# Optimization experiments

Hardware: AMD Instinct MI355X
Metric: run time of the kernel (lower is better)

Reference implementation:

```python
import jax, jax.numpy as jnp
import numpy as np

OUT_FEATURES = 4096
IN_FEATURES = 4096
GROUP_SIZE = 128
N_GROUPS = OUT_FEATURES * IN_FEATURES // GROUP_SIZE  # 131072


def setup_inputs() -> dict:
    key = jax.random.key(0)
    k_x, k_t, k_s = jax.random.split(key, 3)
    x = jax.random.normal(k_x, (4, 2048, IN_FEATURES), dtype=jnp.float32)
    # ternary codes in {-1, 0, 1}, stored as int (int8 in the original module)
    ternary = jax.random.randint(k_t, (OUT_FEATURES, IN_FEATURES), 0, 3, dtype=jnp.int32) - 1
    # per-group positive scales (beta = mean |w| per group in the original init)
    scales = jax.random.uniform(k_s, (N_GROUPS,), dtype=jnp.float32, minval=0.01, maxval=0.1)
    return {"x": x, "ternary": ternary, "scales": scales}


def reference(x, ternary, scales):
    # Dequantize: expand per-group scale across group_size, multiply ternary sign.
    w = (ternary.astype(jnp.float32).reshape(-1, GROUP_SIZE) * scales[:, None])
    w = w.reshape(OUT_FEATURES, IN_FEATURES)
    # F.linear(x, W) = x @ W.T
    return jnp.einsum('bsi,oi->bso', x, w)
```

## Files before the change

kernel.cpp:

```cpp
#include <hip/hip_runtime.h>
#include <hip/hip_bf16.h>


#define Msz 8192
#define Nsz 4096
#define Ksz 4096

typedef __attribute__((ext_vector_type(8))) short short8;
typedef __attribute__((ext_vector_type(4))) float f32x4;
typedef __attribute__((ext_vector_type(4))) int int4v;
typedef __attribute__((ext_vector_type(4))) float float4v;
typedef __attribute__((ext_vector_type(8))) unsigned short ushort8;

static __device__ __forceinline__ unsigned short f2bf(float f) {
    unsigned u = __builtin_bit_cast(unsigned, f);
    u += 0x7fffu + ((u >> 16) & 1u);
    return (unsigned short)(u >> 16);
}

__global__ void prep(const float* __restrict__ x, const int* __restrict__ t,
                     const float* __restrict__ s,
                     unsigned short* __restrict__ ox, unsigned short* __restrict__ ow) {
    if (blockIdx.x < 2048) {
        int i = blockIdx.x * 256 + threadIdx.x;
        for (; i < Msz * Ksz / 8; i += 2048 * 256) {
            const float4v* p = (const float4v*)x + (size_t)i * 2;
            float4v a = p[0], b = p[1];
            ushort8 r;
            r[0] = f2bf(a[0]); r[1] = f2bf(a[1]); r[2] = f2bf(a[2]); r[3] = f2bf(a[3]);
            r[4] = f2bf(b[0]); r[5] = f2bf(b[1]); r[6] = f2bf(b[2]); r[7] = f2bf(b[3]);
            *((ushort8*)ox + i) = r;
        }
    } else {
        int i = (blockIdx.x - 2048) * 256 + threadIdx.x;
        for (; i < Nsz * Ksz / 8; i += 1024 * 256) {
            float sc = s[i >> 4];
            const int4v* p = (const int4v*)t + (size_t)i * 2;
            int4v a = p[0], b = p[1];
            ushort8 r;
            r[0] = f2bf((float)a[0] * sc); r[1] = f2bf((float)a[1] * sc);
            r[2] = f2bf((float)a[2] * sc); r[3] = f2bf((float)a[3] * sc);
            r[4] = f2bf((float)b[0] * sc); r[5] = f2bf((float)b[1] * sc);
            r[6] = f2bf((float)b[2] * sc); r[7] = f2bf((float)b[3] * sc);
            *((ushort8*)ow + i) = r;
        }
    }
}


#define READ_B(b) {                                                              \
    _Pragma("unroll") for (int n = 0; n < 4; ++n)                                \
    _Pragma("unroll") for (int ks = 0; ks < 2; ++ks)                             \
      bfr[n][ks] = *(const short8*)(L + (b)*65536 + 32768 + ((((wc)*4+n)*2+ks)<<10) + laneA); }

#define READ_A(b, q) {                                                           \
    _Pragma("unroll") for (int m = 0; m < 2; ++m)                                \
    _Pragma("unroll") for (int ks = 0; ks < 2; ++ks)                             \
      af[m][ks] = *(const short8*)(L + (b)*65536 + ((((q)*4+(wr)*2+m)*2+ks)<<10) + laneA); }

#define MFMAS(q) {                                                               \
    _Pragma("unroll") for (int m = 0; m < 2; ++m)                                \
    _Pragma("unroll") for (int n = 0; n < 4; ++n) {                              \
      acc[(q)*2+m][n] = __builtin_amdgcn_mfma_f32_16x16x32_bf16(af[m][0], bfr[n][0], acc[(q)*2+m][n], 0, 0, 0); \
      acc[(q)*2+m][n] = __builtin_amdgcn_mfma_f32_16x16x32_bf16(af[m][1], bfr[n][1], acc[(q)*2+m][n], 0, 0, 0); } }

#define STAGE_H(PM, MOFF, BOFF, T, H) {                                          \
    _Pragma("unroll") for (int j = 0; j < 2; ++j)                                \
      __builtin_amdgcn_global_load_lds(                                          \
        (const __attribute__((address_space(1))) void*)(PM + (size_t)((H)*128 + j*64)*Ksz + (T)*64), \
        (__attribute__((address_space(3))) void*)(L + (BOFF) + (MOFF) + (H)*16384 + j*8192 + dOff), \
        16, 0, 0); }

#define WAITV8  asm volatile("s_waitcnt vmcnt(8)"  ::: "memory");
#define WAITV10 asm volatile("s_waitcnt vmcnt(10)" ::: "memory");

#define PHASE(READS, QM, STG, WV)                                                \
    READS;                                                                       \
    STG;                                                                         \
    __builtin_amdgcn_sched_barrier(0);                                           \
    __builtin_amdgcn_s_barrier();                                                \
    asm volatile("s_waitcnt lgkmcnt(0)" ::: "memory");                           \
    __builtin_amdgcn_sched_barrier(0);                                           \
    __builtin_amdgcn_s_setprio(1);                                               \
    MFMAS(QM);                                                                   \
    __builtin_amdgcn_s_setprio(0);                                               \
    WV;                                                                          \
    __builtin_amdgcn_sched_barrier(0);                                           \
    __builtin_amdgcn_s_barrier();                                                \
    __builtin_amdgcn_sched_barrier(0);

__global__ __launch_bounds__(512, 2) void gemm_8p(const unsigned short* __restrict__ A,
                                                  const unsigned short* __restrict__ B,
                                                  float* __restrict__ C) {
    __shared__ __align__(16) unsigned char L[131072];

    const int tid  = threadIdx.x;
    const int lane = tid & 63;
    const int wid  = tid >> 6;
    const int wr   = wid >> 2;
    const int wc   = wid & 3;
    const int rowBase = blockIdx.y * 256;
    const int colBase = blockIdx.x * 256;

    const int laneA = (((lane & 15) * 64) + ((lane >> 4) * 16)) ^ (((lane >> 3) & 1) << 5);
    const int kloc = (lane & 1) * 8 + (((lane >> 1) ^ (lane >> 5)) & 1) * 16;
    const int r_st = lane >> 2;
    const int dOff = wid * 1024;

    const unsigned short* pAb = A + (size_t)(rowBase + (wid >> 1) * 16 + r_st) * Ksz + (wid & 1) * 32 + kloc;
    const unsigned short* pBb = B + (size_t)(colBase + (wid >> 1) * 16 + r_st) * Ksz + (wid & 1) * 32 + kloc;

    f32x4 acc[8][4] = {};
    short8 af[2][2], bfr[4][2];

    STAGE_H(pBb, 32768, 0,     0, 0);
    STAGE_H(pAb, 0,     0,     0, 0);
    STAGE_H(pBb, 32768, 0,     0, 1);
    STAGE_H(pAb, 0,     0,     0, 1);
    STAGE_H(pBb, 32768, 65536, 1, 0);
    STAGE_H(pAb, 0,     65536, 1, 1);
    STAGE_H(pBb, 32768, 65536, 1, 1);
    WAITV8
    __builtin_amdgcn_sched_barrier(0);
    __builtin_amdgcn_s_barrier();
    __builtin_amdgcn_sched_barrier(0);

    for (int i = 0; i < 32; ++i) {
        const int t1 = 2 * i + 1;
        const int t2 = (i < 31) ? 2 * i + 2 : 62;
        const int t3 = (i < 31) ? 2 * i + 3 : 62;

        PHASE({ READ_B(0); READ_A(0, 0); }, 0, STAGE_H(pAb, 0,     65536, t1, 0), )
        PHASE(READ_A(0, 1),                 1, STAGE_H(pBb, 32768, 0,     t2, 0), WAITV10)
        PHASE(READ_A(0, 2),                 2, STAGE_H(pAb, 0,     0,     t2, 0), )
        PHASE(READ_A(0, 3),                 3, STAGE_H(pBb, 32768, 0,     t2, 1), WAITV8)
        PHASE({ READ_B(1); READ_A(1, 2); }, 2, STAGE_H(pAb, 0,     0,     t2, 1), )
        PHASE(READ_A(1, 3),                 3, STAGE_H(pBb, 32768, 65536, t3, 0), WAITV10)
        PHASE(READ_A(1, 0),                 0, STAGE_H(pAb, 0,     65536, t3, 1), )
        PHASE(READ_A(1, 1),                 1, STAGE_H(pBb, 32768, 65536, t3, 1), WAITV8)
    }

    asm volatile("s_waitcnt vmcnt(0)" ::: "memory");

    const int crl = (lane >> 4) * 4;
    const int ccol0 = colBase + wc * 64 + (lane & 15);
#pragma unroll
    for (int q = 0; q < 4; ++q)
#pragma unroll
        for (int m = 0; m < 2; ++m)
#pragma unroll
            for (int n = 0; n < 4; ++n) {
                const int row0 = rowBase + (q * 4 + wr * 2 + m) * 16 + crl;
                float* cp = C + (size_t)row0 * Nsz + ccol0 + n * 16;
#pragma unroll
                for (int j = 0; j < 4; ++j)
                    cp[(size_t)j * Nsz] = acc[q * 2 + m][n][j];
            }
}

__global__ void gemm_naive(const float* __restrict__ x, const int* __restrict__ t,
                           const float* __restrict__ s, float* __restrict__ C) {
    size_t o = (size_t)blockIdx.x * blockDim.x + threadIdx.x;
    if (o >= (size_t)Msz * Nsz) return;
    int m = (int)(o / Nsz), n = (int)(o % Nsz);
    float acc = 0.f;
    for (int g = 0; g < Ksz / 128; ++g) {
        float sc = s[n * (Ksz / 128) + g];
        float p = 0.f;
        const float* xp = x + (size_t)m * Ksz + g * 128;
        const int* tp = t + (size_t)n * Ksz + g * 128;
        for (int k = 0; k < 128; ++k) p += xp[k] * (float)tp[k];
        acc += sc * p;
    }
    C[o] = acc;
}

extern "C" void kernel_launch(void* const* d_in, const int* in_sizes, int n_in,
                              void* d_out, int out_size, void* d_ws, size_t ws_size,
                              hipStream_t stream) {
    const float* x      = (const float*)d_in[0];
    const int*   tern   = (const int*)d_in[1];
    const float* scales = (const float*)d_in[2];
    float* out = (float*)d_out;

    const size_t aBytes = (size_t)Msz * Ksz * 2;
    const size_t bBytes = (size_t)Nsz * Ksz * 2;

    if (ws_size >= aBytes + bBytes) {
        unsigned short* Abf = (unsigned short*)d_ws;
        unsigned short* Bbf = (unsigned short*)((char*)d_ws + aBytes);
        prep<<<3072, 256, 0, stream>>>(x, tern, scales, Abf, Bbf);
        dim3 grid(Nsz / 256, Msz / 256);
        gemm_8p<<<grid, 512, 0, stream>>>(Abf, Bbf, out);
    } else {
        gemm_naive<<<(int)(((size_t)Msz * Nsz + 255) / 256), 256, 0, stream>>>(x, tern, scales, out);
    }
}
```

Before: 266.0 us.

## Double-buffer LDS fragment registers to overlap LDS reads with MFMAs

Splits the A and B fragment registers into even and odd sets, so each phase issues the LDS reads for the next phase while running MFMAs on fragments loaded in the previous phase. The full lgkmcnt(0) wait becomes a partial lgkmcnt wait, and a prologue preloads the first fragments. The goal is to hide LDS read latency behind matrix math. It costs more VGPRs, which could hurt occupancy at launch bounds (512,2). The partial counts also make correctness depend on the vmcnt/lgkmcnt ordering and on the reordered staging slots staying right.

```diff
diff --git a/kernel.cpp b/kernel.cpp
--- a/kernel.cpp
+++ b/kernel.cpp
@@ -48,21 +48,21 @@
 }
 
 
-#define READ_B(b) {                                                              \
+#define READ_B_TO(S, b) {                                                        \
     _Pragma("unroll") for (int n = 0; n < 4; ++n)                                \
     _Pragma("unroll") for (int ks = 0; ks < 2; ++ks)                             \
-      bfr[n][ks] = *(const short8*)(L + (b)*65536 + 32768 + ((((wc)*4+n)*2+ks)<<10) + laneA); }
-
-#define READ_A(b, q) {                                                           \
+      S[n][ks] = *(const short8*)(L + (b)*65536 + 32768 + ((((wc)*4+n)*2+ks)<<10) + laneA); }
+
+#define READ_A_TO(S, b, q) {                                                     \
     _Pragma("unroll") for (int m = 0; m < 2; ++m)                                \
     _Pragma("unroll") for (int ks = 0; ks < 2; ++ks)                             \
-      af[m][ks] = *(const short8*)(L + (b)*65536 + ((((q)*4+(wr)*2+m)*2+ks)<<10) + laneA); }
-
-#define MFMAS(q) {                                                               \
+      S[m][ks] = *(const short8*)(L + (b)*65536 + ((((q)*4+(wr)*2+m)*2+ks)<<10) + laneA); }
+
+#define MFMAS_X(q, AF, BF) {                                                     \
     _Pragma("unroll") for (int m = 0; m < 2; ++m)                                \
     _Pragma("unroll") for (int n = 0; n < 4; ++n) {                              \
-      acc[(q)*2+m][n] = __builtin_amdgcn_mfma_f32_16x16x32_bf16(af[m][0], bfr[n][0], acc[(q)*2+m][n], 0, 0, 0); \
-      acc[(q)*2+m][n] = __builtin_amdgcn_mfma_f32_16x16x32_bf16(af[m][1], bfr[n][1], acc[(q)*2+m][n], 0, 0, 0); } }
+      acc[(q)*2+m][n] = __builtin_amdgcn_mfma_f32_16x16x32_bf16(AF[m][0], BF[n][0], acc[(q)*2+m][n], 0, 0, 0); \
+      acc[(q)*2+m][n] = __builtin_amdgcn_mfma_f32_16x16x32_bf16(AF[m][1], BF[n][1], acc[(q)*2+m][n], 0, 0, 0); } }
 
 #define STAGE_H(PM, MOFF, BOFF, T, H) {                                          \
     _Pragma("unroll") for (int j = 0; j < 2; ++j)                                \
@@ -73,16 +73,18 @@
 
 #define WAITV8  asm volatile("s_waitcnt vmcnt(8)"  ::: "memory");
 #define WAITV10 asm volatile("s_waitcnt vmcnt(10)" ::: "memory");
-
-#define PHASE(READS, QM, STG, WV)                                                \
+#define LG4  asm volatile("s_waitcnt lgkmcnt(4)"  ::: "memory");
+#define LG12 asm volatile("s_waitcnt lgkmcnt(12)" ::: "memory");
+
+#define PHASEP(READS, MF, STG, LG, WV)                                           \
     READS;                                                                       \
     STG;                                                                         \
     __builtin_amdgcn_sched_barrier(0);                                           \
     __builtin_amdgcn_s_barrier();                                                \
-    asm volatile("s_waitcnt lgkmcnt(0)" ::: "memory");                           \
+    LG;                                                                          \
     __builtin_amdgcn_sched_barrier(0);                                           \
     __builtin_amdgcn_s_setprio(1);                                               \
-    MFMAS(QM);                                                                   \
+    MF;                                                                          \
     __builtin_amdgcn_s_setprio(0);                                               \
     WV;                                                                          \
     __builtin_amdgcn_sched_barrier(0);                                           \
@@ -111,7 +113,7 @@
     const unsigned short* pBb = B + (size_t)(colBase + (wid >> 1) * 16 + r_st) * Ksz + (wid & 1) * 32 + kloc;
 
     f32x4 acc[8][4] = {};
-    short8 af[2][2], bfr[4][2];
+    short8 afE[2][2], afO[2][2], bfrE[4][2], bfrO[4][2];
 
     STAGE_H(pBb, 32768, 0,     0, 0);
     STAGE_H(pAb, 0,     0,     0, 0);
@@ -125,22 +127,28 @@
     __builtin_amdgcn_s_barrier();
     __builtin_amdgcn_sched_barrier(0);
 
+    READ_B_TO(bfrE, 0);
+    READ_A_TO(afE, 0, 0);
+    STAGE_H(pAb, 0, 65536, 1, 0);
+    __builtin_amdgcn_sched_barrier(0);
+    __builtin_amdgcn_s_barrier();
+    __builtin_amdgcn_sched_barrier(0);
+
     for (int i = 0; i < 32; ++i) {
-        const int t1 = 2 * i + 1;
         const int t2 = (i < 31) ? 2 * i + 2 : 62;
         const int t3 = (i < 31) ? 2 * i + 3 : 62;
 
-        PHASE({ READ_B(0); READ_A(0, 0); }, 0, STAGE_H(pAb, 0,     65536, t1, 0), )
-        PHASE(READ_A(0, 1),                 1, STAGE_H(pBb, 32768, 0,     t2, 0), WAITV10)
-        PHASE(READ_A(0, 2),                 2, STAGE_H(pAb, 0,     0,     t2, 0), )
-        PHASE(READ_A(0, 3),                 3, STAGE_H(pBb, 32768, 0,     t2, 1), WAITV8)
-        PHASE({ READ_B(1); READ_A(1, 2); }, 2, STAGE_H(pAb, 0,     0,     t2, 1), )
-        PHASE(READ_A(1, 3),                 3, STAGE_H(pBb, 32768, 65536, t3, 0), WAITV10)
-        PHASE(READ_A(1, 0),                 0, STAGE_H(pAb, 0,     65536, t3, 1), )
-        PHASE(READ_A(1, 1),                 1, STAGE_H(pBb, 32768, 65536, t3, 1), WAITV8)
-    }
-
-    asm volatile("s_waitcnt vmcnt(0)" ::: "memory");
+        PHASEP(READ_A_TO(afO, 0, 1),                      MFMAS_X(0, afE, bfrE), STAGE_H(pBb, 32768, 0,     t2, 0), LG4,  WAITV10)
+        PHASEP(READ_A_TO(afE, 0, 2),                      MFMAS_X(1, afO, bfrE), STAGE_H(pAb, 0,     0,     t2, 0), LG4,  )
+        PHASEP(READ_A_TO(afO, 0, 3),                      MFMAS_X(2, afE, bfrE), STAGE_H(pBb, 32768, 0,     t2, 1), LG4,  WAITV8)
+        PHASEP({ READ_B_TO(bfrO, 1); READ_A_TO(afE, 1, 2); }, MFMAS_X(3, afO, bfrE), STAGE_H(pAb, 0,     0,     t2, 1), LG12, )
+        PHASEP(READ_A_TO(afO, 1, 3),                      MFMAS_X(2, afE, bfrO), STAGE_H(pBb, 32768, 65536, t3, 0), LG4,  WAITV10)
+        PHASEP(READ_A_TO(afE, 1, 0),                      MFMAS_X(3, afO, bfrO), STAGE_H(pAb, 0,     65536, t3, 1), LG4,  )
+        PHASEP(READ_A_TO(afO, 1, 1),                      MFMAS_X(0, afE, bfrO), STAGE_H(pBb, 32768, 65536, t3, 1), LG4,  WAITV8)
+        PHASEP({ READ_B_TO(bfrE, 0); READ_A_TO(afE, 0, 0); }, MFMAS_X(1, afO, bfrO), STAGE_H(pAb, 0,     65536, t3, 0), LG12, )
+    }
+
+    asm volatile("s_waitcnt vmcnt(0) lgkmcnt(0)" ::: "memory");
 
     const int crl = (lane >> 4) * 4;
     const int ccol0 = colBase + wc * 64 + (lane & 15);
```

Result: slower. 276.9 us (+4.1%).
